# Optimization experiments

Hardware: AMD Instinct MI355X
Metric: run time of the kernel (lower is better)

Reference implementation:

```python
import jax, jax.numpy as jnp
import numpy as np

D_MODEL = 512
N_HEADS = 8
DEPTH = D_MODEL // N_HEADS
NEG_INF = -1000000000.0


def setup_inputs() -> dict:
    key = jax.random.key(0)
    ks = jax.random.split(key, 12)
    B, S = 4, 2048
    scale = 0.02
    return {
        "Q": jax.random.normal(ks[0], (B, S, D_MODEL), jnp.float32),
        "K": jax.random.normal(ks[1], (B, S, D_MODEL), jnp.float32),
        "V": jax.random.normal(ks[2], (B, S, D_MODEL), jnp.float32),
        "mask": jax.random.randint(ks[3], (B, S, S), 0, 2, jnp.int32),
        "Wq": jax.random.normal(ks[4], (D_MODEL, D_MODEL), jnp.float32) * scale,
        "bq": jnp.zeros((D_MODEL,), jnp.float32),
        "Wk": jax.random.normal(ks[5], (D_MODEL, D_MODEL), jnp.float32) * scale,
        "bk": jnp.zeros((D_MODEL,), jnp.float32),
        "Wv": jax.random.normal(ks[6], (D_MODEL, D_MODEL), jnp.float32) * scale,
        "bv": jnp.zeros((D_MODEL,), jnp.float32),
        "Wo": jax.random.normal(ks[7], (D_MODEL, D_MODEL), jnp.float32) * scale,
        "bo": jnp.zeros((D_MODEL,), jnp.float32),
    }


def _split_heads(x, B):
    # [B, S, d_model] -> [B, H, S, depth]
    S = x.shape[1]
    return x.reshape(B, S, N_HEADS, DEPTH).transpose(0, 2, 1, 3)


def reference(Q, K, V, mask, Wq, bq, Wk, bk, Wv, bv, Wo, bo):
    B, S, _ = Q.shape
    q = _split_heads(Q @ Wq + bq, B)  # [B,H,S,d]
    k = _split_heads(K @ Wk + bk, B)
    v = _split_heads(V @ Wv + bv, B)
    scores = jnp.einsum("bhqd,bhkd->bhqk", q, k) / jnp.sqrt(
        jnp.asarray(DEPTH, jnp.float32))
    m = mask[:, None, :, :]  # broadcast over heads: [B,1,S,S]
    scores = jnp.where(m == 0, jnp.asarray(NEG_INF, scores.dtype), scores)
    attn = jax.nn.softmax(scores, axis=-1)
    ctx = jnp.einsum("bhqk,bhkd->bhqd", attn, v)
    ctx = ctx.transpose(0, 2, 1, 3).reshape(B, S, D_MODEL)
    return ctx @ Wo + bo
```

## Files before the change

### kernel.cpp

```cpp
#include <hip/hip_runtime.h>
#include <hip/hip_bf16.h>
#include <stdint.h>

typedef unsigned short u16;
typedef unsigned int u32;
typedef unsigned long long u64;
using bf16x8 = __attribute__((ext_vector_type(8))) __bf16;
using f32x4  = __attribute__((ext_vector_type(4))) float;
using f32x16 = __attribute__((ext_vector_type(16))) float;

static constexpr int B_ = 4, H_ = 8, S_ = 2048, D_ = 64, DM_ = 512;
#define QSCALE 0.1803368801111601f

__device__ __forceinline__ u16 f2b(float f) {
  u32 u = __float_as_uint(f);
  u = (u + 0x7FFFu + ((u >> 16) & 1u)) >> 16;
  return (u16)u;
}

__device__ __forceinline__ u32 cvtpk_bf16(float a, float b) {
  u32 r;
  asm("v_cvt_pk_bf16_f32 %0, %1, %2" : "=v"(r) : "v"(a), "v"(b));
  return r;
}
__device__ __forceinline__ void plswap(u32& a, u32& b) {
  asm("v_permlane32_swap_b32 %0, %1" : "+v"(a), "+v"(b));
}
__device__ __forceinline__ void gload16(const void* g, void* lds) {
  __builtin_amdgcn_global_load_lds(
      (const __attribute__((address_space(1))) u32*)g,
      (__attribute__((address_space(3))) u32*)lds, 16, 0, 0);
}
#if __has_builtin(__builtin_amdgcn_exp2f)
__device__ __forceinline__ float exp2fast(float x) { return __builtin_amdgcn_exp2f(x); }
#else
__device__ __forceinline__ float exp2fast(float x) {
  float r;
  asm("v_exp_f32 %0, %1" : "=v"(r) : "v"(x));
  return r;
}
#endif

__global__ __launch_bounds__(256) void prep_w_kernel(
    const float* __restrict__ Wq, const float* __restrict__ Wk,
    const float* __restrict__ Wv, const float* __restrict__ Wo,
    u16* __restrict__ Wtq, u16* __restrict__ Wtk, u16* __restrict__ Wtv, u16* __restrict__ Wto) {
  __shared__ float tile[32][33];
  const int z = blockIdx.z;
  const float* W = z == 0 ? Wq : z == 1 ? Wk : z == 2 ? Wv : Wo;
  u16* Wt       = z == 0 ? Wtq : z == 1 ? Wtk : z == 2 ? Wtv : Wto;
  const int k0 = blockIdx.x * 32, n0 = blockIdx.y * 32;
  const int t = threadIdx.x;
  {
    const int kl = t >> 3, nl4 = (t & 7) * 4;
    float4 v = *(const float4*)(W + (size_t)(k0 + kl) * DM_ + n0 + nl4);
    tile[kl][nl4 + 0] = v.x; tile[kl][nl4 + 1] = v.y;
    tile[kl][nl4 + 2] = v.z; tile[kl][nl4 + 3] = v.w;
  }
  __syncthreads();
  {
    const int nl = t >> 3, kl4 = (t & 7) * 4;
    ushort4 o;
    o.x = f2b(tile[kl4 + 0][nl]); o.y = f2b(tile[kl4 + 1][nl]);
    o.z = f2b(tile[kl4 + 2][nl]); o.w = f2b(tile[kl4 + 3][nl]);
    *(ushort4*)(Wt + (size_t)(n0 + nl) * DM_ + k0 + kl4) = o;
  }
}

__global__ void pack_mask_kernel(const int* __restrict__ mask, u32* __restrict__ bits) {
  int i = blockIdx.x * blockDim.x + threadIdx.x;
  unsigned long long bal = __ballot(mask[i] != 0);
  int lane = threadIdx.x & 63;
  if (lane == 0)       bits[i >> 5] = (u32)bal;
  else if (lane == 32) bits[i >> 5] = (u32)(bal >> 32);
}

__global__ __launch_bounds__(256) void gemm_qkv_kernel(
    const float* __restrict__ Qf, const float* __restrict__ Kf, const float* __restrict__ Vf,
    const u16* __restrict__ Wtq, const u16* __restrict__ Wtk, const u16* __restrict__ Wtv,
    const float* __restrict__ bq, const float* __restrict__ bk, const float* __restrict__ bv,
    u16* __restrict__ qp, u16* __restrict__ kp, u16* __restrict__ vp) {
  __shared__ u16 As[128][40];
  __shared__ u16 Bs[128][40];
  const int z = blockIdx.z;
  const float* A    = z == 0 ? Qf : z == 1 ? Kf : Vf;
  const u16* Bt     = z == 0 ? Wtq : z == 1 ? Wtk : Wtv;
  const float* bias = z == 0 ? bq : z == 1 ? bk : bv;
  u16* outp         = z == 0 ? qp : z == 1 ? kp : vp;
  const float scale = z == 0 ? QSCALE : 1.0f;

  const int t = threadIdx.x;
  const int lane = t & 63, wid = t >> 6;
  const int wr = wid >> 1, wc = wid & 1;
  const int l15 = lane & 15, l4 = lane >> 4;
  const int cn = blockIdx.x * 128, rm = blockIdx.y * 128;
  const int srow = t >> 2, scol = (t & 3) << 3;

  f32x4 acc[4][4] = {};

  for (int k0 = 0; k0 < DM_; k0 += 32) {
    __syncthreads();
    {
      const float* a0 = A + (size_t)(rm + srow) * DM_ + k0 + scol;
      float4 f0 = *(const float4*)a0, f1 = *(const float4*)(a0 + 4);
      uint4 u;
      u.x = cvtpk_bf16(f0.x, f0.y); u.y = cvtpk_bf16(f0.z, f0.w);
      u.z = cvtpk_bf16(f1.x, f1.y); u.w = cvtpk_bf16(f1.z, f1.w);
      *(uint4*)(&As[srow][scol]) = u;
      const float* a1 = A + (size_t)(rm + srow + 64) * DM_ + k0 + scol;
      float4 g0 = *(const float4*)a1, g1 = *(const float4*)(a1 + 4);
      uint4 w2;
      w2.x = cvtpk_bf16(g0.x, g0.y); w2.y = cvtpk_bf16(g0.z, g0.w);
      w2.z = cvtpk_bf16(g1.x, g1.y); w2.w = cvtpk_bf16(g1.z, g1.w);
      *(uint4*)(&As[srow + 64][scol]) = w2;
    }
    *(uint4*)(&Bs[srow][scol])      = *(const uint4*)(Bt + (size_t)(cn + srow) * DM_ + k0 + scol);
    *(uint4*)(&Bs[srow + 64][scol]) = *(const uint4*)(Bt + (size_t)(cn + srow + 64) * DM_ + k0 + scol);
    __syncthreads();
    bf16x8 af[4], bfr[4];
#pragma unroll
    for (int m = 0; m < 4; ++m)
      af[m] = *(const bf16x8*)(&As[wr * 64 + m * 16 + l15][l4 * 8]);
#pragma unroll
    for (int n = 0; n < 4; ++n)
      bfr[n] = *(const bf16x8*)(&Bs[wc * 64 + n * 16 + l15][l4 * 8]);
#pragma unroll
    for (int m = 0; m < 4; ++m)
#pragma unroll
      for (int n = 0; n < 4; ++n)
        acc[m][n] = __builtin_amdgcn_mfma_f32_16x16x32_bf16(af[m], bfr[n], acc[m][n], 0, 0, 0);
  }

#pragma unroll
  for (int m = 0; m < 4; ++m)
#pragma unroll
    for (int n = 0; n < 4; ++n) {
      int col = cn + wc * 64 + n * 16 + l15;
      float bv_ = bias[col];
#pragma unroll
      for (int r = 0; r < 4; ++r) {
        int row = rm + wr * 64 + m * 16 + l4 * 4 + r;
        float v = (acc[m][n][r] + bv_) * scale;
        int b = row >> 11, s = row & 2047;
        int h = col >> 6, d = col & 63;
        if (z < 2)
          outp[(((size_t)(b * H_ + h)) * S_ + s) * D_ + d] = f2b(v);
        else
          outp[(((size_t)(b * H_ + h)) * D_ + d) * S_ + s] = f2b(v);
      }
    }
}

__global__ __launch_bounds__(256) void gemm_out_kernel(
    const u16* __restrict__ A, const u16* __restrict__ Bt,
    const float* __restrict__ bias, float* __restrict__ outp) {
  __shared__ u16 As[64][40];
  __shared__ u16 Bs[128][40];
  const int t = threadIdx.x;
  const int lane = t & 63, w = t >> 6;
  const int l15 = lane & 15, l4 = lane >> 4;
  const int cn = blockIdx.x * 128, rm = blockIdx.y * 64;
  const int srow = t >> 2, scol = (t & 3) << 3;

  f32x4 acc[4][2] = {};

  for (int k0 = 0; k0 < DM_; k0 += 32) {
    __syncthreads();
    *(uint4*)(&As[srow][scol])      = *(const uint4*)(A + (size_t)(rm + srow) * DM_ + k0 + scol);
    *(uint4*)(&Bs[srow][scol])      = *(const uint4*)(Bt + (size_t)(cn + srow) * DM_ + k0 + scol);
    *(uint4*)(&Bs[srow + 64][scol]) = *(const uint4*)(Bt + (size_t)(cn + srow + 64) * DM_ + k0 + scol);
    __syncthreads();
    bf16x8 af[4], bfr[2];
#pragma unroll
    for (int m = 0; m < 4; ++m)
      af[m] = *(const bf16x8*)(&As[m * 16 + l15][l4 * 8]);
#pragma unroll
    for (int n = 0; n < 2; ++n)
      bfr[n] = *(const bf16x8*)(&Bs[w * 32 + n * 16 + l15][l4 * 8]);
#pragma unroll
    for (int m = 0; m < 4; ++m)
#pragma unroll
      for (int n = 0; n < 2; ++n)
        acc[m][n] = __builtin_amdgcn_mfma_f32_16x16x32_bf16(af[m], bfr[n], acc[m][n], 0, 0, 0);
  }

#pragma unroll
  for (int m = 0; m < 4; ++m)
#pragma unroll
    for (int n = 0; n < 2; ++n) {
      int col = cn + w * 32 + n * 16 + l15;
      float bv_ = bias[col];
#pragma unroll
      for (int r = 0; r < 4; ++r) {
        int row = rm + m * 16 + l4 * 4 + r;
        outp[(size_t)row * DM_ + col] = acc[m][n][r] + bv_;
      }
    }
}

__global__ __launch_bounds__(256, 4) void attn_kernel(
    const u16* __restrict__ qp, const u16* __restrict__ kp, const u16* __restrict__ vp,
    const u64* __restrict__ mbits, u16* __restrict__ ctx) {
  __shared__ __align__(16) char smem[32768];
  const int t = threadIdx.x, lane = t & 63, w = t >> 6;
  const int l31 = lane & 31, hi = lane >> 5;
  const int ksub = w & 1, qsub = w >> 1;
  const int wgid = blockIdx.x;
  const int h = wgid & 7, idx = wgid >> 3;
  const int b = idx >> 5, qt = idx & 31;
  const size_t head  = ((size_t)(b * H_ + h)) * S_ * D_;
  const size_t headT = ((size_t)(b * H_ + h)) * D_ * S_;
  const int q0 = qt * 64 + qsub * 32;
  const int q  = q0 + l31;

  bf16x8 qf[4];
  {
    const u16* qrow = qp + head + (size_t)q * D_;
#pragma unroll
    for (int ks = 0; ks < 4; ++ks) qf[ks] = *(const bf16x8*)(qrow + ks * 16 + hi * 8);
  }

  const int kxor = (l31 & 7) << 4;
  const int krbase = (ksub * 32 + l31) * 128;
  const int rbase0 = l31 * 128, rbase1 = (32 + l31) * 128;
  int colx[4];
#pragma unroll
  for (int s = 0; s < 4; ++s) colx[s] = ((s * 32 + hi * 16) ^ kxor);
  int vcolx[2];
#pragma unroll
  for (int s = 0; s < 2; ++s) vcolx[s] = ((ksub * 64 + s * 32 + hi * 16) ^ kxor);

  const int srow = lane >> 3;
  const int scol = ((lane & 7) ^ srow) << 3;
  const int c0 = w, c1 = w + 4;
  const u16* ksrc0 = kp + head + (size_t)(c0 * 8 + srow) * D_ + scol;
  const u16* ksrc1 = kp + head + (size_t)(c1 * 8 + srow) * D_ + scol;
  const u16* vsrc0 = vp + headT + (size_t)(c0 * 8 + srow) * S_ + scol;
  const u16* vsrc1 = vp + headT + (size_t)(c1 * 8 + srow) * S_ + scol;

  f32x16 accO0, accO1;
#pragma unroll
  for (int i = 0; i < 16; ++i) { accO0[i] = 0.f; accO1[i] = 0.f; }
  float lrow = 0.f;

  const u64* mrowp = mbits + ((size_t)b * S_ + q) * (S_ / 64);

  auto stage = [&](int bufi, int kt) {
    char* kb = smem + bufi * 8192;
    char* vb = smem + 16384 + bufi * 8192;
    gload16(ksrc0 + (size_t)kt * 4096, kb + c0 * 1024);
    gload16(ksrc1 + (size_t)kt * 4096, kb + c1 * 1024);
    gload16(vsrc0 + kt * 64, vb + c0 * 1024);
    gload16(vsrc1 + kt * 64, vb + c1 * 1024);
  };

  stage(0, 0);
  __syncthreads();
  int buf = 0;

  for (int kt = 0; kt < S_ / 64; ++kt) {
    if (kt < S_ / 64 - 1) stage(buf ^ 1, kt + 1);
    const u32 m32 = (u32)(mrowp[kt] >> (ksub * 32 + hi * 4));

    const char* kb = smem + buf * 8192;
    const char* vb = smem + 16384 + buf * 8192;

    f32x16 s;
#pragma unroll
    for (int i = 0; i < 16; ++i) s[i] = 0.f;
    {
      bf16x8 kf[4];
#pragma unroll
      for (int ks = 0; ks < 4; ++ks) kf[ks] = *(const bf16x8*)(kb + krbase + colx[ks]);
      __builtin_amdgcn_s_setprio(1);
#pragma unroll
      for (int ks = 0; ks < 4; ++ks)
        s = __builtin_amdgcn_mfma_f32_32x32x16_bf16(kf[ks], qf[ks], s, 0, 0, 0);
      __builtin_amdgcn_s_setprio(0);
    }

    float e[16];
    float rs[4] = {0.f, 0.f, 0.f, 0.f};
#pragma unroll
    for (int r = 0; r < 16; ++r) {
      const int kbit = (r & 3) + 8 * (r >> 2);
      float ex = exp2fast(s[r]);
      ex = ((m32 >> kbit) & 1u) ? ex : 0.f;
      e[r] = ex;
      rs[r & 3] += ex;
    }
    float rsum = (rs[0] + rs[1]) + (rs[2] + rs[3]);
    rsum += __shfl_xor(rsum, 32);
    lrow += rsum;

    {
      u32 pw[8];
#pragma unroll
      for (int j = 0; j < 8; ++j)
        pw[j] = cvtpk_bf16(e[2 * j], e[2 * j + 1]);
      plswap(pw[0], pw[2]); plswap(pw[1], pw[3]);
      plswap(pw[4], pw[6]); plswap(pw[5], pw[7]);
      __builtin_amdgcn_s_setprio(1);
#pragma unroll
      for (int s2 = 0; s2 < 2; ++s2) {
        union { u32 wds[4]; bf16x8 v; } pa;
        pa.wds[0] = pw[s2 * 4 + 0]; pa.wds[1] = pw[s2 * 4 + 1];
        pa.wds[2] = pw[s2 * 4 + 2]; pa.wds[3] = pw[s2 * 4 + 3];
        bf16x8 vf0 = *(const bf16x8*)(vb + rbase0 + vcolx[s2]);
        accO0 = __builtin_amdgcn_mfma_f32_32x32x16_bf16(pa.v, vf0, accO0, 0, 0, 0);
        bf16x8 vf1 = *(const bf16x8*)(vb + rbase1 + vcolx[s2]);
        accO1 = __builtin_amdgcn_mfma_f32_32x32x16_bf16(pa.v, vf1, accO1, 0, 0, 0);
      }
      __builtin_amdgcn_s_setprio(0);
    }
    __syncthreads();
    buf ^= 1;
  }

  float (*Ol)[32][64] = (float (*)[32][64])smem;
  float* Ll = (float*)(smem + 16384);
  if (ksub == 1) {
#pragma unroll
    for (int r = 0; r < 16; ++r) {
      const int qr = (r & 3) + 8 * (r >> 2) + 4 * hi;
      Ol[qsub][qr][l31]      = accO0[r];
      Ol[qsub][qr][32 + l31] = accO1[r];
    }
    if (hi == 0) Ll[qsub * 32 + l31] = lrow;
  }
  __syncthreads();
  if (ksub == 0) {
    lrow += Ll[qsub * 32 + l31];
    float inv = 1.0f / lrow;
    float invr[16];
#pragma unroll
    for (int r = 0; r < 16; ++r) invr[r] = __shfl(inv, (r & 3) + 8 * (r >> 2) + 4 * hi);

    const int colA = h * 64 + l31, colB = h * 64 + 32 + l31;
#pragma unroll
    for (int r = 0; r < 16; ++r) {
      const int qr = (r & 3) + 8 * (r >> 2) + 4 * hi;
      const int row = q0 + qr;
      u16* o = ctx + ((size_t)(b * S_) + row) * DM_;
      o[colA] = f2b((accO0[r] + Ol[qsub][qr][l31])      * invr[r]);
      o[colB] = f2b((accO1[r] + Ol[qsub][qr][32 + l31]) * invr[r]);
    }
  }
}

extern "C" void kernel_launch(void* const* d_in, const int* in_sizes, int n_in,
                              void* d_out, int out_size, void* d_ws, size_t ws_size,
                              hipStream_t stream) {
  const float* Q  = (const float*)d_in[0];
  const float* K  = (const float*)d_in[1];
  const float* V  = (const float*)d_in[2];
  const int* mask = (const int*)d_in[3];
  const float* Wq = (const float*)d_in[4];
  const float* bq = (const float*)d_in[5];
  const float* Wk = (const float*)d_in[6];
  const float* bk = (const float*)d_in[7];
  const float* Wv = (const float*)d_in[8];
  const float* bv = (const float*)d_in[9];
  const float* Wo = (const float*)d_in[10];
  const float* bo = (const float*)d_in[11];

  char* ws = (char*)d_ws;
  size_t off = 0;
  auto alloc = [&](size_t bytes) -> void* {
    void* p = ws + off;
    off += (bytes + 255) & ~(size_t)255;
    return p;
  };
  const size_t act_b = (size_t)B_ * S_ * DM_ * 2;
  u16* Wtq = (u16*)alloc((size_t)DM_ * DM_ * 2);
  u16* Wtk = (u16*)alloc((size_t)DM_ * DM_ * 2);
  u16* Wtv = (u16*)alloc((size_t)DM_ * DM_ * 2);
  u16* Wto = (u16*)alloc((size_t)DM_ * DM_ * 2);
  u32* mbits = (u32*)alloc((size_t)B_ * S_ * (S_ / 32) * 4);
  u16* qp  = (u16*)alloc(act_b);
  u16* kp  = (u16*)alloc(act_b);
  u16* vp  = (u16*)alloc(act_b);
  u16* ctx = (u16*)alloc(act_b);

  prep_w_kernel<<<dim3(16, 16, 4), 256, 0, stream>>>(Wq, Wk, Wv, Wo, Wtq, Wtk, Wtv, Wto);
  pack_mask_kernel<<<(B_ * S_ * S_) / 256, 256, 0, stream>>>(mask, mbits);

  gemm_qkv_kernel<<<dim3(4, 64, 3), 256, 0, stream>>>(
      Q, K, V, Wtq, Wtk, Wtv, bq, bk, bv, qp, kp, vp);

  attn_kernel<<<dim3(1024), 256, 0, stream>>>(qp, kp, vp, (const u64*)mbits, ctx);

  gemm_out_kernel<<<dim3(4, 128), 256, 0, stream>>>(ctx, Wto, bo, (float*)d_out);
}
```

Baseline: 146.6 us.

## Pre-swizzle mask into per-wave ballot layout for scalar-register select in attention

The mask packing kernel now transposes 32x64 mask tiles through shared memory and emits 64-bit wave-wide ballots already arranged to match the MFMA output register layout. The attention kernel loads 16 uniform u64 masks per key tile and applies them with v_cndmask using an SGPR predicate, which removes the per-lane shift/and/select work. It also seeds the first MFMA with a zero accumulator instead of zeroing the score registers each iteration. The cost is 16 scalar loads per tile per wave and a more complex packing kernel that uses shared memory.

```diff
diff --git a/kernel.cpp b/kernel.cpp
--- a/kernel.cpp
+++ b/kernel.cpp
@@ -40,6 +40,11 @@
   return r;
 }
 #endif
+__device__ __forceinline__ float selmask(float ex, u64 pred) {
+  float r;
+  asm("v_cndmask_b32 %0, 0, %1, %2" : "=v"(r) : "v"(ex), "s"(pred));
+  return r;
+}
 
 __global__ __launch_bounds__(256) void prep_w_kernel(
     const float* __restrict__ Wq, const float* __restrict__ Wk,
@@ -67,12 +72,24 @@
   }
 }
 
-__global__ void pack_mask_kernel(const int* __restrict__ mask, u32* __restrict__ bits) {
-  int i = blockIdx.x * blockDim.x + threadIdx.x;
-  unsigned long long bal = __ballot(mask[i] != 0);
-  int lane = threadIdx.x & 63;
-  if (lane == 0)       bits[i >> 5] = (u32)bal;
-  else if (lane == 32) bits[i >> 5] = (u32)(bal >> 32);
+__global__ __launch_bounds__(256) void pack_mask_kernel(const int* __restrict__ mask,
+                                                        u64* __restrict__ wmask) {
+  __shared__ int mt[4][32][65];
+  const int t = threadIdx.x, lane = t & 63, w = t >> 6;
+  const int kt = blockIdx.x * 4 + w, qg = blockIdx.y, b = blockIdx.z;
+  const int q0 = qg * 32;
+  const int* src = mask + ((size_t)b * S_ + q0) * S_ + kt * 64 + lane;
+#pragma unroll 8
+  for (int i = 0; i < 32; ++i) mt[w][i][lane] = src[(size_t)i * S_];
+  u64* dst = wmask + (((size_t)(b * 64 + qg) * 32 + kt) * 32);
+  const int hi4 = (lane >> 5) * 4;
+#pragma unroll
+  for (int idx = 0; idx < 32; ++idx) {
+    const int ksub = idx >> 4, r = idx & 15;
+    const int key = ksub * 32 + (r & 3) + 8 * (r >> 2) + hi4;
+    u64 bal = __ballot(mt[w][lane & 31][key] != 0);
+    if (lane == 0) dst[idx] = bal;
+  }
 }
 
 __global__ __launch_bounds__(256) void gemm_qkv_kernel(
@@ -200,11 +217,12 @@
 
 __global__ __launch_bounds__(256, 4) void attn_kernel(
     const u16* __restrict__ qp, const u16* __restrict__ kp, const u16* __restrict__ vp,
-    const u64* __restrict__ mbits, u16* __restrict__ ctx) {
+    const u64* __restrict__ wmask, u16* __restrict__ ctx) {
   __shared__ __align__(16) char smem[32768];
   const int t = threadIdx.x, lane = t & 63, w = t >> 6;
   const int l31 = lane & 31, hi = lane >> 5;
   const int ksub = w & 1, qsub = w >> 1;
+  const int wu = __builtin_amdgcn_readfirstlane(w);
   const int wgid = blockIdx.x;
   const int h = wgid & 7, idx = wgid >> 3;
   const int b = idx >> 5, qt = idx & 31;
@@ -220,6 +238,8 @@
     for (int ks = 0; ks < 4; ++ks) qf[ks] = *(const bf16x8*)(qrow + ks * 16 + hi * 8);
   }
 
+  const u64* wm = wmask + (((size_t)(b * 64 + qt * 2 + (wu >> 1)) * 32) * 32) + (wu & 1) * 16;
+
   const int kxor = (l31 & 7) << 4;
   const int krbase = (ksub * 32 + l31) * 128;
   const int rbase0 = l31 * 128, rbase1 = (32 + l31) * 128;
@@ -238,12 +258,10 @@
   const u16* vsrc0 = vp + headT + (size_t)(c0 * 8 + srow) * S_ + scol;
   const u16* vsrc1 = vp + headT + (size_t)(c1 * 8 + srow) * S_ + scol;
 
-  f32x16 accO0, accO1;
-#pragma unroll
-  for (int i = 0; i < 16; ++i) { accO0[i] = 0.f; accO1[i] = 0.f; }
+  f32x16 accO0, accO1, FZ;
+#pragma unroll
+  for (int i = 0; i < 16; ++i) { accO0[i] = 0.f; accO1[i] = 0.f; FZ[i] = 0.f; }
   float lrow = 0.f;
-
-  const u64* mrowp = mbits + ((size_t)b * S_ + q) * (S_ / 64);
 
   auto stage = [&](int bufi, int kt) {
     char* kb = smem + bufi * 8192;
@@ -260,21 +278,25 @@
 
   for (int kt = 0; kt < S_ / 64; ++kt) {
     if (kt < S_ / 64 - 1) stage(buf ^ 1, kt + 1);
-    const u32 m32 = (u32)(mrowp[kt] >> (ksub * 32 + hi * 4));
+    u64 mskr[16];
+    {
+      const u64* wmk = wm + kt * 32;
+#pragma unroll
+      for (int r = 0; r < 16; ++r) mskr[r] = wmk[r];
+    }
 
     const char* kb = smem + buf * 8192;
     const char* vb = smem + 16384 + buf * 8192;
 
     f32x16 s;
-#pragma unroll
-    for (int i = 0; i < 16; ++i) s[i] = 0.f;
     {
       bf16x8 kf[4];
 #pragma unroll
       for (int ks = 0; ks < 4; ++ks) kf[ks] = *(const bf16x8*)(kb + krbase + colx[ks]);
       __builtin_amdgcn_s_setprio(1);
-#pragma unroll
-      for (int ks = 0; ks < 4; ++ks)
+      s = __builtin_amdgcn_mfma_f32_32x32x16_bf16(kf[0], qf[0], FZ, 0, 0, 0);
+#pragma unroll
+      for (int ks = 1; ks < 4; ++ks)
         s = __builtin_amdgcn_mfma_f32_32x32x16_bf16(kf[ks], qf[ks], s, 0, 0, 0);
       __builtin_amdgcn_s_setprio(0);
     }
@@ -283,11 +305,9 @@
     float rs[4] = {0.f, 0.f, 0.f, 0.f};
 #pragma unroll
     for (int r = 0; r < 16; ++r) {
-      const int kbit = (r & 3) + 8 * (r >> 2);
-      float ex = exp2fast(s[r]);
-      ex = ((m32 >> kbit) & 1u) ? ex : 0.f;
-      e[r] = ex;
-      rs[r & 3] += ex;
+      float em = selmask(exp2fast(s[r]), mskr[r]);
+      e[r] = em;
+      rs[r & 3] += em;
     }
     float rsum = (rs[0] + rs[1]) + (rs[2] + rs[3]);
     rsum += __shfl_xor(rsum, 32);
@@ -376,19 +396,19 @@
   u16* Wtk = (u16*)alloc((size_t)DM_ * DM_ * 2);
   u16* Wtv = (u16*)alloc((size_t)DM_ * DM_ * 2);
   u16* Wto = (u16*)alloc((size_t)DM_ * DM_ * 2);
-  u32* mbits = (u32*)alloc((size_t)B_ * S_ * (S_ / 32) * 4);
+  u64* wmask = (u64*)alloc((size_t)B_ * 64 * 32 * 32 * 8);
   u16* qp  = (u16*)alloc(act_b);
   u16* kp  = (u16*)alloc(act_b);
   u16* vp  = (u16*)alloc(act_b);
   u16* ctx = (u16*)alloc(act_b);
 
   prep_w_kernel<<<dim3(16, 16, 4), 256, 0, stream>>>(Wq, Wk, Wv, Wo, Wtq, Wtk, Wtv, Wto);
-  pack_mask_kernel<<<(B_ * S_ * S_) / 256, 256, 0, stream>>>(mask, mbits);
+  pack_mask_kernel<<<dim3(8, 64, 4), 256, 0, stream>>>(mask, wmask);
 
   gemm_qkv_kernel<<<dim3(4, 64, 3), 256, 0, stream>>>(
       Q, K, V, Wtq, Wtk, Wtv, bq, bk, bv, qp, kp, vp);
 
-  attn_kernel<<<dim3(1024), 256, 0, stream>>>(qp, kp, vp, (const u64*)mbits, ctx);
+  attn_kernel<<<dim3(1024), 256, 0, stream>>>(qp, kp, vp, wmask, ctx);
 
   gemm_out_kernel<<<dim3(4, 128), 256, 0, stream>>>(ctx, Wto, bo, (float*)d_out);
 }
```

Result: faster. 129.1 us (-11.9%).
